# Optimization experiments

Measured on AMD Instinct MI355X. Metric: run time of the kernel, lower is better.

The kernel has to match this reference:

```python
import jax, jax.numpy as jnp
import numpy as np
from functools import partial

T, B, CH, H, W = 16, 4, 128, 128, 128
TAU, VTH, ALPHA, EPS = 2.0, 1.0, 2.0, 1e-5

# ATan surrogate-gradient spike (spikingjelly surrogate.ATan, alpha=2.0)
@jax.custom_vjp
def spike(x):
    return (x >= 0.0).astype(x.dtype)

def _spike_fwd(x):
    return spike(x), x

def _spike_bwd(x, g):
    return (g * (ALPHA / 2.0) / (1.0 + (jnp.pi / 2.0 * ALPHA * x) ** 2),)

spike.defvjp(_spike_fwd, _spike_bwd)

def _conv(x, w):  # x [N,C,H,W], w [O,I,3,3], padding=1 -> SAME
    return jax.lax.conv_general_dilated(x, w, (1, 1), 'SAME',
                                        dimension_numbers=('NCHW', 'OIHW', 'NCHW'))

def _bn(x, g, b, m, v):  # inference-mode BatchNorm2d, channel axis 1
    inv = g / jnp.sqrt(v + EPS)
    return x * inv[:, None, None] + (b - m * inv)[:, None, None]

def _pool(x):  # MaxPool2d(2,2), NCHW
    return jax.lax.reduce_window(x, -jnp.inf, jax.lax.max,
                                 (1, 1, 2, 2), (1, 1, 2, 2), 'VALID')

def _lif(xs):  # xs [T, ...]; LIFNode: tau=2, v_th=1, v_reset=0, decay_input, hard reset (detached)
    def step(v, x):
        v = v + (x - v) / TAU                      # charge
        s = spike(v - VTH)                         # fire (Heaviside fwd, ATan bwd)
        v = v * (1.0 - jax.lax.stop_gradient(s))   # detached hard reset to 0
        return v, s
    return jax.lax.scan(step, jnp.zeros_like(xs[0]), xs)[1]

def _block(xs, w, g, b, m, v):  # conv -> BN -> LIF -> maxpool, xs [T,B,C,H,W]
    t, bs = xs.shape[0], xs.shape[1]
    y = _bn(_conv(xs.reshape((t * bs,) + xs.shape[2:]), w), g, b, m, v)
    y = _lif(y.reshape((t, bs) + y.shape[1:]))
    y = _pool(y.reshape((t * bs,) + y.shape[2:]))
    return y.reshape((t, bs) + y.shape[1:])


def setup_inputs() -> dict:
    key = jax.random.key(0)
    ks = jax.random.split(key, 8)
    inp = {'x': jax.random.uniform(ks[0], (T, B, 2, H, W), jnp.float32)}
    fan_ins = [2 * 9, CH * 9, CH * 9, CH * 9]
    for i in range(4):
        cin = 2 if i == 0 else CH
        inp[f'w{i+1}'] = jax.random.normal(ks[i + 1], (CH, cin, 3, 3), jnp.float32) * np.sqrt(2.0 / fan_ins[i]).astype(np.float32)
        inp[f'g{i+1}'] = jnp.ones((CH,), jnp.float32)
        inp[f'b{i+1}'] = jnp.zeros((CH,), jnp.float32)
        inp[f'm{i+1}'] = jnp.zeros((CH,), jnp.float32)
        inp[f'v{i+1}'] = jnp.ones((CH,), jnp.float32)
    inp['wfc'] = jax.random.normal(ks[5], (10, CH * 8 * 8), jnp.float32) * np.sqrt(1.0 / (CH * 64)).astype(np.float32)
    inp['bfc'] = jnp.zeros((10,), jnp.float32)
    return inp


def reference(x, w1, g1, b1, m1, v1, w2, g2, b2, m2, v2,
              w3, g3, b3, m3, v3, w4, g4, b4, m4, v4, wfc, bfc):
    y = _block(x, w1, g1, b1, m1, v1)   # [T,B,CH,64,64]
    y = _block(y, w2, g2, b2, m2, v2)   # [T,B,CH,32,32]
    y = _block(y, w3, g3, b3, m3, v3)   # [T,B,CH,16,16]
    y = _block(y, w4, g4, b4, m4, v4)   # [T,B,CH,8,8]
    z = y.reshape(y.shape[0], y.shape[1], -1) @ wfc.T + bfc  # [T,B,10]
    return _lif(z)                       # output spike train [T,B,10]
```

## Files before the change

kernel.cpp:

```cpp
#include <hip/hip_runtime.h>
#include <hip/hip_bf16.h>
#include <math.h>

#define T_STEPS 16
#define BATCH 4
#define NCH 128

typedef __attribute__((ext_vector_type(8))) short bf16x8;
typedef __attribute__((ext_vector_type(4))) float f32x4;

__global__ __launch_bounds__(256) void transpose_w_kernel(const float* __restrict__ w,
                                                          float* __restrict__ wT, int rows) {
  int idx = blockIdx.x * 256 + threadIdx.x;
  if (idx < rows * 128) {
    int r = idx >> 7, co = idx & 127;
    wT[idx] = w[co * rows + r];
  }
}

__global__ __launch_bounds__(256) void prep_w_kernel(const float* __restrict__ w,
                                                     __hip_bfloat16* __restrict__ wp) {
  int idx = blockIdx.x * 256 + threadIdx.x;
  if (idx >= 147456) return;
  int co = idx / 1152, rem = idx - co * 1152;
  int ci = rem / 9, tap = rem - ci * 9;
  float x = w[idx];
  float h = (float)__float2bfloat16(x);
  float r1 = x - h;
  float m = (float)__float2bfloat16(r1);
  float r2 = r1 - m;
  float l = (float)__float2bfloat16(r2);
  size_t base = ((size_t)tap * 128 + co) * 128 + ci;
  wp[base] = __float2bfloat16(h);
  wp[147456 + base] = __float2bfloat16(m);
  wp[294912 + base] = __float2bfloat16(l);
}

__global__ __launch_bounds__(256) void layer1_kernel(
    const float* __restrict__ x, const float* __restrict__ wT,
    const float* __restrict__ gn, const float* __restrict__ bn,
    const float* __restrict__ mn, const float* __restrict__ vn,
    __hip_bfloat16* __restrict__ out) {
  const int tid = threadIdx.x;
  const int quad = tid & 15;
  const int qy = (quad >> 2) << 1, qx = (quad & 3) << 1;
  const int coi = tid >> 4;
  const int cob = blockIdx.y * 64;
  const int co0 = cob + coi * 4;
  const int tile = blockIdx.x;
  const int ty0 = (tile >> 4) << 3, tx0 = (tile & 15) << 3;
  const int b = blockIdx.z;

  __shared__ float Wl[18 * 64];
  __shared__ float Il[2 * 100];

  for (int idx = tid; idx < 18 * 64; idx += 256) {
    int r = idx >> 6, c = idx & 63;
    Wl[idx] = wT[r * 128 + cob + c];
  }

  float scale[4], shift[4];
#pragma unroll
  for (int j = 0; j < 4; ++j) {
    float inv = gn[co0 + j] / sqrtf(vn[co0 + j] + 1e-5f);
    scale[j] = inv;
    shift[j] = bn[co0 + j] - mn[co0 + j] * inv;
  }

  float vm[4][4];
#pragma unroll
  for (int j = 0; j < 4; ++j)
#pragma unroll
    for (int p = 0; p < 4; ++p) vm[j][p] = 0.f;

  for (int t = 0; t < T_STEPS; ++t) {
    __syncthreads();
    const float* xt = x + (size_t)((t * BATCH + b) * 2) * 16384;
    for (int idx = tid; idx < 200; idx += 256) {
      int ci = idx / 100, rem = idx - ci * 100;
      int y = rem / 10, xx = rem - y * 10;
      int gy = ty0 - 1 + y, gx = tx0 - 1 + xx;
      float val = 0.f;
      if ((unsigned)gy < 128u && (unsigned)gx < 128u)
        val = xt[ci * 16384 + gy * 128 + gx];
      Il[idx] = val;
    }
    __syncthreads();

    float acc[4][4];
#pragma unroll
    for (int j = 0; j < 4; ++j)
#pragma unroll
      for (int p = 0; p < 4; ++p) acc[j][p] = 0.f;

    for (int ci = 0; ci < 2; ++ci) {
      float iv[4][4];
#pragma unroll
      for (int r = 0; r < 4; ++r)
#pragma unroll
        for (int c = 0; c < 4; ++c) iv[r][c] = Il[ci * 100 + (qy + r) * 10 + (qx + c)];
#pragma unroll
      for (int k = 0; k < 9; ++k) {
        const int dy = k / 3, dx = k - (k / 3) * 3;
        float w0 = Wl[(ci * 9 + k) * 64 + coi * 4 + 0];
        float w1 = Wl[(ci * 9 + k) * 64 + coi * 4 + 1];
        float w2 = Wl[(ci * 9 + k) * 64 + coi * 4 + 2];
        float w3 = Wl[(ci * 9 + k) * 64 + coi * 4 + 3];
#pragma unroll
        for (int sy = 0; sy < 2; ++sy)
#pragma unroll
          for (int sx = 0; sx < 2; ++sx) {
            float xin = iv[sy + dy][sx + dx];
            acc[0][sy * 2 + sx] += w0 * xin;
            acc[1][sy * 2 + sx] += w1 * xin;
            acc[2][sy * 2 + sx] += w2 * xin;
            acc[3][sy * 2 + sx] += w3 * xin;
          }
      }
    }

    const int py = (ty0 >> 1) + (quad >> 2);
    const int px = (tx0 >> 1) + (quad & 3);
#pragma unroll
    for (int j = 0; j < 4; ++j) {
      float pooled = 0.f;
#pragma unroll
      for (int p = 0; p < 4; ++p) {
        float yv = acc[j][p] * scale[j] + shift[j];
        float nv = vm[j][p] + (yv - vm[j][p]) * 0.5f;
        float s = (nv >= 1.0f) ? 1.0f : 0.0f;
        pooled = fmaxf(pooled, s);
        vm[j][p] = (nv >= 1.0f) ? 0.f : nv;
      }
      out[(((size_t)(t * BATCH + b) * 64 + py) * 64 + px) * 128 + co0 + j] =
          __float2bfloat16(pooled);
    }
  }
}

template <int S>
__global__ __launch_bounds__(512) void conv_mfma_kernel(
    const __hip_bfloat16* __restrict__ spk, const __hip_bfloat16* __restrict__ wp,
    float* __restrict__ pre, int t_base) {
  constexpr int TILES_X = S / 8;
  const int tile = blockIdx.x;
  const int ty0 = (tile / TILES_X) * 16;
  const int tx0 = (tile % TILES_X) * 8;
  const int tbl = blockIdx.z;
  const int tbg = t_base * 4 + tbl;
  const int tid = threadIdx.x;
  const int lane = tid & 63;
  const int wid = tid >> 6;

  __shared__ alignas(16) unsigned char At[46080];

  const __hip_bfloat16* sp = spk + (size_t)tbg * S * S * 128;
  for (int c = tid; c < 2880; c += 512) {
    int y = c / 160, rem = c - y * 160;
    int xx = rem >> 4, cg = rem & 15;
    int gy = ty0 - 1 + y, gx = tx0 - 1 + xx;
    uint4 v = make_uint4(0u, 0u, 0u, 0u);
    if ((unsigned)gy < (unsigned)S && (unsigned)gx < (unsigned)S)
      v = *(const uint4*)(sp + ((size_t)(gy * S + gx)) * 128 + cg * 8);
    *(uint4*)(At + (y * 10 + xx) * 256 + ((cg ^ (xx & 7)) * 16)) = v;
  }
  __syncthreads();

  f32x4 acc[8] = {};

  const int g = lane >> 4;
  const int co0 = wid * 16 + (lane & 15);
  const short* wb = (const short*)wp + (size_t)co0 * 128 + g * 8;
  const int lx = lane & 7;
  const int lh = (lane >> 3) & 1;

  for (int tap = 0; tap < 9; ++tap) {
    const int dy = tap / 3, dx = tap - dy * 3;
    const int xx = lx + dx;
    const int xoff = xx * 256;
    const int ybase = lh + dy;
#pragma unroll
    for (int kk = 0; kk < 4; ++kk) {
      bf16x8 a[8];
      const int slot = ((kk * 4 + g) ^ (xx & 7)) * 16;
#pragma unroll
      for (int m = 0; m < 8; ++m)
        a[m] = *(const bf16x8*)(At + (2 * m + ybase) * 2560 + xoff + slot);
#pragma unroll
      for (int s = 0; s < 3; ++s) {
        bf16x8 b = *(const bf16x8*)(wb + (size_t)(s * 9 + tap) * 16384 + kk * 32);
#pragma unroll
        for (int m = 0; m < 8; ++m)
          acc[m] = __builtin_amdgcn_mfma_f32_16x16x32_bf16(a[m], b, acc[m], 0, 0, 0);
      }
    }
  }

  const int rr = (lane >> 4) * 4;
  float* po = pre + (size_t)tbl * S * S * 128 + co0;
#pragma unroll
  for (int m = 0; m < 8; ++m) {
#pragma unroll
    for (int j = 0; j < 4; ++j) {
      int p = m * 16 + rr + j;
      int py = p >> 3, px = p & 7;
      po[((size_t)(ty0 + py) * S + tx0 + px) * 128] = acc[m][j];
    }
  }
}

template <int S>
__global__ __launch_bounds__(256) void lif_pool_kernel(
    const float* __restrict__ pre, __hip_bfloat16* __restrict__ spk,
    float* __restrict__ vm, const float* __restrict__ gn,
    const float* __restrict__ bn, const float* __restrict__ mn,
    const float* __restrict__ vn, int t_base, int nt) {
  constexpr int OS = S / 2, NQ = OS * OS;
  const int tid = threadIdx.x;
  const int co = tid & 127;
  const int q = blockIdx.x * 2 + (tid >> 7);
  const int b = blockIdx.z;
  const int qy = q / OS, qx = q - qy * OS;
  float inv = gn[co] / sqrtf(vn[co] + 1e-5f);
  float sc = inv, sh = bn[co] - mn[co] * inv;
  float* vp = vm + (((size_t)b * NQ + q) * 4) * 128 + co;
  float v0, v1, v2, v3;
  if (t_base == 0) {
    v0 = v1 = v2 = v3 = 0.f;
  } else {
    v0 = vp[0]; v1 = vp[128]; v2 = vp[256]; v3 = vp[384];
  }
  const size_t rowstride = (size_t)S * 128;
  for (int t = 0; t < nt; ++t) {
    const float* p = pre + (((size_t)(t * 4 + b) * S + qy * 2) * S + qx * 2) * 128 + co;
    float x00 = p[0] * sc + sh;
    float x01 = p[128] * sc + sh;
    float x10 = p[rowstride] * sc + sh;
    float x11 = p[rowstride + 128] * sc + sh;
    float n0 = v0 + (x00 - v0) * 0.5f; float s0 = n0 >= 1.f ? 1.f : 0.f; v0 = n0 >= 1.f ? 0.f : n0;
    float n1 = v1 + (x01 - v1) * 0.5f; float s1 = n1 >= 1.f ? 1.f : 0.f; v1 = n1 >= 1.f ? 0.f : n1;
    float n2 = v2 + (x10 - v2) * 0.5f; float s2 = n2 >= 1.f ? 1.f : 0.f; v2 = n2 >= 1.f ? 0.f : n2;
    float n3 = v3 + (x11 - v3) * 0.5f; float s3 = n3 >= 1.f ? 1.f : 0.f; v3 = n3 >= 1.f ? 0.f : n3;
    float pooled = fmaxf(fmaxf(s0, s1), fmaxf(s2, s3));
    spk[((size_t)((t_base + t) * 4 + b) * NQ + q) * 128 + co] = __float2bfloat16(pooled);
  }
  if (t_base + nt < T_STEPS) {
    vp[0] = v0; vp[128] = v1; vp[256] = v2; vp[384] = v3;
  }
}

__global__ __launch_bounds__(256) void fc_kernel(const __hip_bfloat16* __restrict__ a4,
                                                 const float* __restrict__ wfc,
                                                 const float* __restrict__ bfc,
                                                 float* __restrict__ z) {
  const int tb = blockIdx.x;
  const int tid = threadIdx.x;
  const __hip_bfloat16* a = a4 + (size_t)tb * 8192;
  float part[10];
#pragma unroll
  for (int o = 0; o < 10; ++o) part[o] = 0.f;
  for (int i = tid; i < 8192; i += 256) {
    int co = i >> 6, yx = i & 63;
    float av = __bfloat162float(a[yx * 128 + co]);
#pragma unroll
    for (int o = 0; o < 10; ++o) part[o] += av * wfc[o * 8192 + i];
  }
#pragma unroll
  for (int o = 0; o < 10; ++o)
    for (int off = 32; off > 0; off >>= 1) part[o] += __shfl_xor(part[o], off, 64);
  __shared__ float red[4][10];
  if ((tid & 63) == 0) {
#pragma unroll
    for (int o = 0; o < 10; ++o) red[tid >> 6][o] = part[o];
  }
  __syncthreads();
  if (tid < 10)
    z[tb * 10 + tid] = red[0][tid] + red[1][tid] + red[2][tid] + red[3][tid] + bfc[tid];
}

__global__ void out_lif_kernel(const float* __restrict__ z, float* __restrict__ out) {
  int i = threadIdx.x;
  if (i < 40) {
    float v = 0.f;
    for (int t = 0; t < T_STEPS; ++t) {
      float yv = z[t * 40 + i];
      float nv = v + (yv - v) * 0.5f;
      float s = (nv >= 1.0f) ? 1.0f : 0.0f;
      out[t * 40 + i] = s;
      v = (nv >= 1.0f) ? 0.f : nv;
    }
  }
}

extern "C" void kernel_launch(void* const* d_in, const int* in_sizes, int n_in,
                              void* d_out, int out_size, void* d_ws, size_t ws_size,
                              hipStream_t stream) {
  const float* x = (const float*)d_in[0];
  const float* w1 = (const float*)d_in[1];
  const float* g1 = (const float*)d_in[2];
  const float* b1 = (const float*)d_in[3];
  const float* m1 = (const float*)d_in[4];
  const float* v1 = (const float*)d_in[5];
  const float* w2 = (const float*)d_in[6];
  const float* g2 = (const float*)d_in[7];
  const float* b2 = (const float*)d_in[8];
  const float* m2 = (const float*)d_in[9];
  const float* v2 = (const float*)d_in[10];
  const float* w3 = (const float*)d_in[11];
  const float* g3 = (const float*)d_in[12];
  const float* b3 = (const float*)d_in[13];
  const float* m3 = (const float*)d_in[14];
  const float* v3 = (const float*)d_in[15];
  const float* w4 = (const float*)d_in[16];
  const float* g4 = (const float*)d_in[17];
  const float* b4 = (const float*)d_in[18];
  const float* m4 = (const float*)d_in[19];
  const float* v4 = (const float*)d_in[20];
  const float* wfc = (const float*)d_in[21];
  const float* bfc = (const float*)d_in[22];
  float* out = (float*)d_out;

  float* p = (float*)d_ws;
  float* wT1 = p; p += 2304;
  __hip_bfloat16* wp2 = (__hip_bfloat16*)p; p += 221184;
  __hip_bfloat16* wp3 = (__hip_bfloat16*)p; p += 221184;
  __hip_bfloat16* wp4 = (__hip_bfloat16*)p; p += 221184;
  __hip_bfloat16* spk1 = (__hip_bfloat16*)p; p += 16777216;
  float* preH = p; p += 16777216;
  __hip_bfloat16* spk2 = (__hip_bfloat16*)p; p += 4194304;
  float* vm2 = p; p += 2097152;
  __hip_bfloat16* spk3 = (__hip_bfloat16*)p; p += 1048576;
  float* vm3 = p; p += 524288;
  __hip_bfloat16* spk4 = (__hip_bfloat16*)p; p += 262144;
  float* vm4 = p; p += 131072;
  float* z = p; p += 640;

  transpose_w_kernel<<<9, 256, 0, stream>>>(w1, wT1, 18);
  prep_w_kernel<<<576, 256, 0, stream>>>(w2, wp2);
  prep_w_kernel<<<576, 256, 0, stream>>>(w3, wp3);
  prep_w_kernel<<<576, 256, 0, stream>>>(w4, wp4);

  layer1_kernel<<<dim3(256, 2, 4), 256, 0, stream>>>(x, wT1, g1, b1, m1, v1, spk1);

  conv_mfma_kernel<64><<<dim3(32, 1, 32), 512, 0, stream>>>(spk1, wp2, preH, 0);
  lif_pool_kernel<64><<<dim3(512, 1, 4), 256, 0, stream>>>(preH, spk2, vm2, g2, b2, m2, v2, 0, 8);
  conv_mfma_kernel<64><<<dim3(32, 1, 32), 512, 0, stream>>>(spk1, wp2, preH, 8);
  lif_pool_kernel<64><<<dim3(512, 1, 4), 256, 0, stream>>>(preH, spk2, vm2, g2, b2, m2, v2, 8, 8);

  conv_mfma_kernel<32><<<dim3(8, 1, 64), 512, 0, stream>>>(spk2, wp3, preH, 0);
  lif_pool_kernel<32><<<dim3(128, 1, 4), 256, 0, stream>>>(preH, spk3, vm3, g3, b3, m3, v3, 0, 16);

  conv_mfma_kernel<16><<<dim3(2, 1, 64), 512, 0, stream>>>(spk3, wp4, preH, 0);
  lif_pool_kernel<16><<<dim3(32, 1, 4), 256, 0, stream>>>(preH, spk4, vm4, g4, b4, m4, v4, 0, 16);

  fc_kernel<<<64, 256, 0, stream>>>(spk4, wfc, bfc, z);
  out_lif_kernel<<<1, 64, 0, stream>>>(z, out);
}
```

Before: 520.8 us.

## Restructure layer1 conv: weights in registers, larger spatial tiles, vector stores

The layer-1 kernel is remapped so each block handles 4 output channels over a 32x32 spatial tile instead of 64 channels over an 8x8 tile. Each thread keeps its 72 weights in registers, so the shared-memory weight staging and the separate transpose kernel are no longer needed. The four bf16 channel outputs are packed into a single short4 store. In exchange, every block re-reads a 34x34 input halo, and x is read 32 times across channel groups instead of twice, while the stores become 8-byte writes strided at 256 bytes.

```diff
diff --git a/kernel.cpp b/kernel.cpp
--- a/kernel.cpp
+++ b/kernel.cpp
@@ -8,15 +8,6 @@
 
 typedef __attribute__((ext_vector_type(8))) short bf16x8;
 typedef __attribute__((ext_vector_type(4))) float f32x4;
-
-__global__ __launch_bounds__(256) void transpose_w_kernel(const float* __restrict__ w,
-                                                          float* __restrict__ wT, int rows) {
-  int idx = blockIdx.x * 256 + threadIdx.x;
-  if (idx < rows * 128) {
-    int r = idx >> 7, co = idx & 127;
-    wT[idx] = w[co * rows + r];
-  }
-}
 
 __global__ __launch_bounds__(256) void prep_w_kernel(const float* __restrict__ w,
                                                      __hip_bfloat16* __restrict__ wp) {
@@ -37,27 +28,26 @@
 }
 
 __global__ __launch_bounds__(256) void layer1_kernel(
-    const float* __restrict__ x, const float* __restrict__ wT,
+    const float* __restrict__ x, const float* __restrict__ w,
     const float* __restrict__ gn, const float* __restrict__ bn,
     const float* __restrict__ mn, const float* __restrict__ vn,
     __hip_bfloat16* __restrict__ out) {
   const int tid = threadIdx.x;
-  const int quad = tid & 15;
-  const int qy = (quad >> 2) << 1, qx = (quad & 3) << 1;
-  const int coi = tid >> 4;
-  const int cob = blockIdx.y * 64;
-  const int co0 = cob + coi * 4;
   const int tile = blockIdx.x;
-  const int ty0 = (tile >> 4) << 3, tx0 = (tile & 15) << 3;
+  const int ty0 = (tile >> 2) * 32, tx0 = (tile & 3) * 32;
+  const int co0 = blockIdx.y * 4;
   const int b = blockIdx.z;
-
-  __shared__ float Wl[18 * 64];
-  __shared__ float Il[2 * 100];
-
-  for (int idx = tid; idx < 18 * 64; idx += 256) {
-    int r = idx >> 6, c = idx & 63;
-    Wl[idx] = wT[r * 128 + cob + c];
-  }
+  const int qx2 = (tid & 15) * 2;
+  const int qy2 = (tid >> 4) * 2;
+
+  float wreg[2][9][4];
+#pragma unroll
+  for (int j = 0; j < 4; ++j)
+#pragma unroll
+    for (int ci = 0; ci < 2; ++ci)
+#pragma unroll
+      for (int tap = 0; tap < 9; ++tap)
+        wreg[ci][tap][j] = w[(co0 + j) * 18 + ci * 9 + tap];
 
   float scale[4], shift[4];
 #pragma unroll
@@ -73,12 +63,14 @@
 #pragma unroll
     for (int p = 0; p < 4; ++p) vm[j][p] = 0.f;
 
+  __shared__ float Il[2 * 34 * 34];
+
   for (int t = 0; t < T_STEPS; ++t) {
     __syncthreads();
     const float* xt = x + (size_t)((t * BATCH + b) * 2) * 16384;
-    for (int idx = tid; idx < 200; idx += 256) {
-      int ci = idx / 100, rem = idx - ci * 100;
-      int y = rem / 10, xx = rem - y * 10;
+    for (int idx = tid; idx < 2312; idx += 256) {
+      int ci = idx / 1156, rem = idx - ci * 1156;
+      int y = rem / 34, xx = rem - y * 34;
       int gy = ty0 - 1 + y, gx = tx0 - 1 + xx;
       float val = 0.f;
       if ((unsigned)gy < 128u && (unsigned)gx < 128u)
@@ -93,34 +85,33 @@
 #pragma unroll
       for (int p = 0; p < 4; ++p) acc[j][p] = 0.f;
 
+#pragma unroll
     for (int ci = 0; ci < 2; ++ci) {
       float iv[4][4];
 #pragma unroll
       for (int r = 0; r < 4; ++r)
 #pragma unroll
-        for (int c = 0; c < 4; ++c) iv[r][c] = Il[ci * 100 + (qy + r) * 10 + (qx + c)];
-#pragma unroll
-      for (int k = 0; k < 9; ++k) {
-        const int dy = k / 3, dx = k - (k / 3) * 3;
-        float w0 = Wl[(ci * 9 + k) * 64 + coi * 4 + 0];
-        float w1 = Wl[(ci * 9 + k) * 64 + coi * 4 + 1];
-        float w2 = Wl[(ci * 9 + k) * 64 + coi * 4 + 2];
-        float w3 = Wl[(ci * 9 + k) * 64 + coi * 4 + 3];
+        for (int c = 0; c < 4; ++c) iv[r][c] = Il[ci * 1156 + (qy2 + r) * 34 + qx2 + c];
+#pragma unroll
+      for (int tap = 0; tap < 9; ++tap) {
+        const int dy = tap / 3, dx = tap - dy * 3;
 #pragma unroll
         for (int sy = 0; sy < 2; ++sy)
 #pragma unroll
           for (int sx = 0; sx < 2; ++sx) {
             float xin = iv[sy + dy][sx + dx];
-            acc[0][sy * 2 + sx] += w0 * xin;
-            acc[1][sy * 2 + sx] += w1 * xin;
-            acc[2][sy * 2 + sx] += w2 * xin;
-            acc[3][sy * 2 + sx] += w3 * xin;
+            acc[0][sy * 2 + sx] += wreg[ci][tap][0] * xin;
+            acc[1][sy * 2 + sx] += wreg[ci][tap][1] * xin;
+            acc[2][sy * 2 + sx] += wreg[ci][tap][2] * xin;
+            acc[3][sy * 2 + sx] += wreg[ci][tap][3] * xin;
           }
       }
     }
 
-    const int py = (ty0 >> 1) + (quad >> 2);
-    const int px = (tx0 >> 1) + (quad & 3);
+    const int py = (ty0 >> 1) + (tid >> 4);
+    const int px = (tx0 >> 1) + (tid & 15);
+    short4 pk;
+    short* pks = (short*)&pk;
 #pragma unroll
     for (int j = 0; j < 4; ++j) {
       float pooled = 0.f;
@@ -132,9 +123,10 @@
         pooled = fmaxf(pooled, s);
         vm[j][p] = (nv >= 1.0f) ? 0.f : nv;
       }
-      out[(((size_t)(t * BATCH + b) * 64 + py) * 64 + px) * 128 + co0 + j] =
-          __float2bfloat16(pooled);
-    }
+      __hip_bfloat16 bv = __float2bfloat16(pooled);
+      pks[j] = *(short*)&bv;
+    }
+    *(short4*)(out + (((size_t)(t * BATCH + b) * 64 + py) * 64 + px) * 128 + co0) = pk;
   }
 }
 
@@ -321,7 +313,6 @@
   float* out = (float*)d_out;
 
   float* p = (float*)d_ws;
-  float* wT1 = p; p += 2304;
   __hip_bfloat16* wp2 = (__hip_bfloat16*)p; p += 221184;
   __hip_bfloat16* wp3 = (__hip_bfloat16*)p; p += 221184;
   __hip_bfloat16* wp4 = (__hip_bfloat16*)p; p += 221184;
@@ -335,12 +326,11 @@
   float* vm4 = p; p += 131072;
   float* z = p; p += 640;
 
-  transpose_w_kernel<<<9, 256, 0, stream>>>(w1, wT1, 18);
   prep_w_kernel<<<576, 256, 0, stream>>>(w2, wp2);
   prep_w_kernel<<<576, 256, 0, stream>>>(w3, wp3);
   prep_w_kernel<<<576, 256, 0, stream>>>(w4, wp4);
 
-  layer1_kernel<<<dim3(256, 2, 4), 256, 0, stream>>>(x, wT1, g1, b1, m1, v1, spk1);
+  layer1_kernel<<<dim3(16, 32, 4), 256, 0, stream>>>(x, w1, g1, b1, m1, v1, spk1);
 
   conv_mfma_kernel<64><<<dim3(32, 1, 32), 512, 0, stream>>>(spk1, wp2, preH, 0);
   lif_pool_kernel<64><<<dim3(512, 1, 4), 256, 0, stream>>>(preH, spk2, vm2, g2, b2, m2, v2, 0, 8);
```

New measurement: 571.4 us. +9.7%, slower.
